# Kernel optimization log

Hardware: AMD Instinct MI355X
Metric: run time of the kernel (lower is better)

The kernel has to match this reference:

```python
import jax, jax.numpy as jnp
import numpy as np

N_FFT = 1024
HOP = 256
WIN = N_FFT  # win_length = n_fft in VocosISTFTHead
PAD = (WIN - HOP) // 2  # 384, 'same' padding trim
CLAMP_MAX = 100.0


def _hann_periodic(n):
    # matches torch.hann_window(n, periodic=True)
    return 0.5 * (1.0 - jnp.cos(2.0 * jnp.pi * jnp.arange(n, dtype=jnp.float32) / n))


def setup_inputs() -> dict:
    key = jax.random.key(0)
    k1, k2, k3 = jax.random.split(key, 3)
    B, T, H = 16, 2048, 512
    hidden_states = jax.random.normal(k1, (B, T, H), dtype=jnp.float32)
    # out_proj: Linear(hidden_dim, n_fft+2); scaled so exp(magnitude) stays sane
    W = jax.random.normal(k2, (N_FFT + 2, H), dtype=jnp.float32) * 0.02
    b = jax.random.normal(k3, (N_FFT + 2,), dtype=jnp.float32) * 0.02
    window = _hann_periodic(WIN)
    return {"hidden_states": hidden_states, "W": W, "b": b, "window": window}


def reference(hidden_states, W, b, window):
    B, T, _ = hidden_states.shape
    # linear projection -> [B, T, n_fft+2] -> transpose -> [B, n_fft+2, T]
    spec = (hidden_states @ W.T + b).transpose(0, 2, 1)
    half = (N_FFT + 2) // 2  # n_fft//2 + 1 = 513 freq bins
    magnitude = jnp.minimum(jnp.exp(spec[:, :half]), CLAMP_MAX)
    phase = spec[:, half:]
    coeffs = magnitude * (jnp.cos(phase) + 1j * jnp.sin(phase))  # [B, F, T] complex
    # inverse rfft along freq axis, norm='backward' (default) -> [B, n_fft, T]
    frames = jnp.fft.irfft(coeffs, n=N_FFT, axis=1)
    frames = frames * window[None, :, None]
    L = (T - 1) * HOP + WIN
    idx = (jnp.arange(T)[:, None] * HOP + jnp.arange(WIN)[None, :]).reshape(-1)
    frames_flat = frames.transpose(0, 2, 1).reshape(B, -1)
    audio = jnp.zeros((B, L), frames.dtype).at[:, idx].add(frames_flat)
    # NOLA normalization: overlap-added squared window
    wsq = jnp.broadcast_to(window ** 2, (T, WIN)).reshape(-1)
    norm = jnp.zeros((L,), window.dtype).at[idx].add(wsq)
    return audio[:, PAD:-PAD] / norm[PAD:-PAD]
```

## Files before the change

### kernel.cpp

```cpp
#include <hip/hip_runtime.h>
#include <hip/hip_fp16.h>
#include <math.h>
#include <stdint.h>


#define FRAMES  32768
#define TWO_PI  6.283185307179586f
#define SPR 4
#define RND 11
#define JB  47

typedef unsigned short ushort_t;
typedef __attribute__((ext_vector_type(8))) _Float16 f16x8;
typedef __attribute__((ext_vector_type(4))) float f32x4;

#define GLDS(gp, lp) __builtin_amdgcn_global_load_lds( \
    (const __attribute__((address_space(1))) void*)(gp), \
    (__attribute__((address_space(3))) void*)(lp), 16, 0, 0)

__device__ __forceinline__ float2 f2(float x, float y){ return make_float2(x,y); }
__device__ __forceinline__ float2 cadd(float2 a, float2 b){ return f2(a.x+b.x, a.y+b.y); }
__device__ __forceinline__ float2 csub(float2 a, float2 b){ return f2(a.x-b.x, a.y-b.y); }
__device__ __forceinline__ float2 cmul(float2 a, float2 b){ return f2(a.x*b.x - a.y*b.y, a.x*b.y + a.y*b.x); }

__device__ __forceinline__ uint32_t pack2h(float a, float b) {
  const ushort_t ha = __half_as_ushort(__float2half_rn(a));
  const ushort_t hb = __half_as_ushort(__float2half_rn(b));
  return (uint32_t)ha | ((uint32_t)hb << 16);
}

__global__ __launch_bounds__(256) void convert_AB(
    const float* __restrict__ hs, const float* __restrict__ Wm,
    const float* __restrict__ bias, ushort_t* __restrict__ Af,
    ushort_t* __restrict__ Whi, __half* __restrict__ coeffs)
{
  const int bid = blockIdx.x;
  const int t = threadIdx.x;
  if (bid < 2048) {
    const int r = t >> 4, c = t & 15;
    const int m = bid * 16 + r;
    const float* src = hs + (size_t)m * 512 + c * 32;
    const float* wm  = Wm + (size_t)512  * 512 + c * 32;
    const float* wp  = Wm + (size_t)1025 * 512 + c * 32;

    float v[32];
    #pragma unroll
    for (int i = 0; i < 8; ++i) *(float4*)&v[i*4] = *(const float4*)(src + i*4);

    float dm = 0.f, dp = 0.f;
    #pragma unroll
    for (int i = 0; i < 8; ++i) {
      const float4 a  = *(const float4*)&v[i*4];
      const float4 m4 = *(const float4*)(wm + i*4);
      const float4 p4 = *(const float4*)(wp + i*4);
      dm = fmaf(a.x,m4.x, fmaf(a.y,m4.y, fmaf(a.z,m4.z, fmaf(a.w,m4.w, dm))));
      dp = fmaf(a.x,p4.x, fmaf(a.y,p4.y, fmaf(a.z,p4.z, fmaf(a.w,p4.w, dp))));
    }

    uint32_t hu[16];
    #pragma unroll
    for (int i = 0; i < 16; ++i) hu[i] = pack2h(v[2*i], v[2*i+1]);
    ushort_t* dh = Af + (size_t)m * 512 + c * 32;
    #pragma unroll
    for (int q = 0; q < 4; ++q)
      *(uint4*)(dh + q*8) = make_uint4(hu[4*q], hu[4*q+1], hu[4*q+2], hu[4*q+3]);

    #pragma unroll
    for (int off = 8; off; off >>= 1) {
      dm += __shfl_xor(dm, off, 16);
      dp += __shfl_xor(dp, off, 16);
    }
    if (c == 0) {
      const float sm = dm + bias[512], sp = dp + bias[1025];
      const float mag = fminf(__expf(sm), 100.0f);
      coeffs[(size_t)m * 1024 + 1] = __float2half_rn(mag * __cosf(sp));
    }
  } else {
    const int gid = (bid - 2048) * 256 + t;
    const int sd = gid & 3;
    const int r  = (gid >> 2) & 255;
    const int kt = (gid >> 10) & 15;
    const int yb = gid >> 14;
    const int srow = (r < 128) ? (yb*128 + r) : (513 + yb*128 + (r - 128));
    const float* src = Wm + (size_t)srow * 512 + kt*32 + sd*8;
    const float4 a = *(const float4*)src;
    const float4 b = *(const float4*)(src + 4);
    const uint4 o = make_uint4(pack2h(a.x,a.y), pack2h(a.z,a.w),
                               pack2h(b.x,b.y), pack2h(b.z,b.w));
    *(uint4*)(Whi + (size_t)gid * 8) = o;
  }
}

__global__ __launch_bounds__(512, 2) void gemm_mfma(
    const ushort_t* __restrict__ Af, const ushort_t* __restrict__ Whi,
    const float* __restrict__ bias, __half* __restrict__ coeffs)
{
  __shared__ ushort_t Ab[24576];

  const int tid = threadIdx.x;
  const int w = tid >> 6, l = tid & 63;
  const int wr = w >> 2, wc = w & 3;
  const int lc = l & 15, kg = l >> 4;

  const int bid = blockIdx.x;
  const int swz = (bid & 7) * 64 + (bid >> 3);
  const int mb = swz >> 2, yb = swz & 3;

  uint32_t pa_off[2], lofs[2];
  #pragma unroll
  for (int ch = 0; ch < 2; ++ch) {
    const int g = ch*512 + tid;
    const int r = g >> 2, sd = g & 3;
    lofs[ch] = r*32 + sd*8;
    const int sl = sd ^ ((r >> 1) & 3);
    pa_off[ch] = (uint32_t)(mb*256 + r)*512 + sl*8;
  }
  uint32_t pb_off[4];
  #pragma unroll
  for (int cf = 0; cf < 4; ++cf) {
    const int rB = ((cf < 2) ? 0 : 128) + wc*32 + (cf & 1)*16 + lc;
    pb_off[cf] = (uint32_t)yb*131072u + rB*32 + kg*8;
  }

  f32x4 acc[8][4];
  #pragma unroll
  for (int rf = 0; rf < 8; ++rf)
    #pragma unroll
    for (int cf = 0; cf < 4; ++cf)
      #pragma unroll
      for (int q = 0; q < 4; ++q) acc[rf][cf][q] = 0.f;

  const int asl = (kg ^ ((lc >> 1) & 3)) * 8;

  f16x8 p[4], q[4];

#define WAITV2 asm volatile("s_waitcnt vmcnt(2) lgkmcnt(0)" ::: "memory")
#define WAITV0 asm volatile("s_waitcnt vmcnt(0) lgkmcnt(0)" ::: "memory")
#define SB     __builtin_amdgcn_s_barrier()
#define SCH0   __builtin_amdgcn_sched_barrier(0)

#define DSREAD(DST, BASE, RF0) do {                                      \
    _Pragma("unroll")                                                    \
    for (int r4 = 0; r4 < 4; ++r4) {                                     \
      const int rr = wr*128 + ((RF0) + r4)*16 + lc;                      \
      DST[r4] = *(const f16x8*)(&Ab[(BASE) + rr*32 + asl]);              \
    }                                                                    \
  } while (0)

#define MFMA16(FA, RF0, RB) do {                                         \
    __builtin_amdgcn_s_setprio(1);                                       \
    _Pragma("unroll")                                                    \
    for (int r4 = 0; r4 < 4; ++r4)                                       \
      _Pragma("unroll")                                                  \
      for (int cf = 0; cf < 4; ++cf)                                     \
        acc[(RF0)+r4][cf] = __builtin_amdgcn_mfma_f32_16x16x32_f16(      \
            FA[r4], RB[cf], acc[(RF0)+r4][cf], 0, 0, 0);                 \
    __builtin_amdgcn_s_setprio(0);                                       \
  } while (0)

#define ITER(KT, RBC, RBN, LAST) do {                                    \
    if (LAST) { WAITV0; } else { WAITV2; }                               \
    SB;                                                                  \
    DSREAD(q, aR, 4);                                                    \
    if ((KT) < 14) GLDS(Af + pa_off[0] + ((KT)+2)*32, &Ab[aW + lofs[0]]);\
    if ((KT) < 15) {                                                     \
      RBN[0] = *(const f16x8*)(Whi + pb_off[0] + ((KT)+1)*8192);         \
      RBN[1] = *(const f16x8*)(Whi + pb_off[1] + ((KT)+1)*8192);         \
    }                                                                    \
    SCH0;                                                                \
    MFMA16(p, 0, RBC);                                                   \
    if ((KT) < 15) DSREAD(p, aN, 0);                                     \
    if ((KT) < 14) GLDS(Af + pa_off[1] + ((KT)+2)*32, &Ab[aW + lofs[1]]);\
    if ((KT) < 15) {                                                     \
      RBN[2] = *(const f16x8*)(Whi + pb_off[2] + ((KT)+1)*8192);         \
      RBN[3] = *(const f16x8*)(Whi + pb_off[3] + ((KT)+1)*8192);         \
    }                                                                    \
    SCH0;                                                                \
    MFMA16(q, 4, RBC);                                                   \
    { const unsigned t_ = aR; aR = aN; aN = aW; aW = t_; }               \
  } while (0)

  f16x8 rb0[4], rb1[4];
  GLDS(Af + pa_off[0], &Ab[lofs[0]]);
  GLDS(Af + pa_off[1], &Ab[lofs[1]]);
  GLDS(Af + pa_off[0] + 32, &Ab[8192 + lofs[0]]);
  GLDS(Af + pa_off[1] + 32, &Ab[8192 + lofs[1]]);
  SCH0;
  #pragma unroll
  for (int j = 0; j < 4; ++j) rb0[j] = *(const f16x8*)(Whi + pb_off[j]);
  SCH0;
  asm volatile("s_waitcnt vmcnt(6)" ::: "memory");
  SB;
  unsigned aR = 0, aN = 8192, aW = 16384;
  DSREAD(p, aR, 0);

  for (int k2 = 0; k2 < 8; ++k2) {
    ITER(2*k2,     rb0, rb1, false);
    ITER(2*k2 + 1, rb1, rb0, k2 == 7);
  }
#undef ITER
#undef DSREAD
#undef MFMA16

  const int pc0 = yb*128 + wc*32 + lc;
  const int pc1 = pc0 + 16;
  const float bm0 = bias[pc0], bp0 = bias[513 + pc0];
  const float bm1 = bias[pc1], bp1 = bias[513 + pc1];
  #pragma unroll
  for (int rf = 0; rf < 8; ++rf) {
    const int rbase = mb*256 + wr*128 + rf*16 + kg*4;
    #pragma unroll
    for (int qi = 0; qi < 4; ++qi) {
      __half* row = coeffs + (size_t)(rbase + qi) * 1024;
      {
        const float sm = acc[rf][0][qi] + bm0;
        const float sp = acc[rf][2][qi] + bp0;
        const float mag = fminf(__expf(sm), 100.0f);
        const float aa = mag * __cosf(sp);
        const float bb = mag * __sinf(sp);
        if (pc0 == 0) row[0] = __float2half_rn(aa);
        else *(__half2*)(row + 2*pc0) = __float22half2_rn(make_float2(aa, bb));
      }
      {
        const float sm = acc[rf][1][qi] + bm1;
        const float sp = acc[rf][3][qi] + bp1;
        const float mag = fminf(__expf(sm), 100.0f);
        const float aa = mag * __cosf(sp);
        const float bb = mag * __sinf(sp);
        *(__half2*)(row + 2*pc1) = __float22half2_rn(make_float2(aa, bb));
      }
    }
  }
}

#define PIDX(s) ((s) + ((s) >> 3))
#define WFENCE  __builtin_amdgcn_wave_barrier()

template<int NS>
__device__ __forceinline__ void stage_fft(const float2* in, float2* out, int l)
{
  float2 v[8];
  #pragma unroll
  for (int r = 0; r < 8; ++r) v[r] = in[PIDX(l + 64*r)];
  if (NS > 1) {
    const float ang = TWO_PI * (float)(l & (NS-1)) / (float)(NS * 8);
    float sn, cs; __sincosf(ang, &sn, &cs);
    const float2 wb = f2(cs, sn);
    float2 cur = wb;
    #pragma unroll
    for (int r = 1; r < 8; ++r) { v[r] = cmul(v[r], cur); cur = cmul(cur, wb); }
  }
  const float2 e0=v[0], e1=v[2], e2=v[4], e3=v[6];
  const float2 o0=v[1], o1=v[3], o2=v[5], o3=v[7];
  float2 a = cadd(e0,e2), b = csub(e0,e2), c = cadd(e1,e3), d = csub(e1,e3);
  const float2 E0 = cadd(a,c), E2 = csub(a,c);
  const float2 E1 = f2(b.x - d.y, b.y + d.x), E3 = f2(b.x + d.y, b.y - d.x);
  a = cadd(o0,o2); b = csub(o0,o2); c = cadd(o1,o3); d = csub(o1,o3);
  const float2 O0 = cadd(a,c), O2 = csub(a,c);
  const float2 O1 = f2(b.x - d.y, b.y + d.x), O3 = f2(b.x + d.y, b.y - d.x);
  const float r2 = 0.70710678118654752f;
  const float2 t0 = O0;
  const float2 t1 = f2(r2*(O1.x - O1.y),  r2*(O1.x + O1.y));
  const float2 t2 = f2(-O2.y, O2.x);
  const float2 t3 = f2(-r2*(O3.x + O3.y), r2*(O3.x - O3.y));
  float2 X[8];
  X[0]=cadd(E0,t0); X[4]=csub(E0,t0);
  X[1]=cadd(E1,t1); X[5]=csub(E1,t1);
  X[2]=cadd(E2,t2); X[6]=csub(E2,t2);
  X[3]=cadd(E3,t3); X[7]=csub(E3,t3);
  const int idxD = (l / NS) * (NS * 8) + (l & (NS-1));
  #pragma unroll
  for (int q = 0; q < 8; ++q) out[PIDX(idxD + q*NS)] = X[q];
}

__device__ __forceinline__ void stage_last(const float2* in, __half* frout,
                                           const float* __restrict__ window, int l)
{
  float2 v[8];
  #pragma unroll
  for (int r = 0; r < 8; ++r) v[r] = in[PIDX(l + 64*r)];
  {
    const float ang = TWO_PI * (float)l / 512.0f;
    float sn, cs; __sincosf(ang, &sn, &cs);
    const float2 wb = f2(cs, sn);
    float2 cur = wb;
    #pragma unroll
    for (int r = 1; r < 8; ++r) { v[r] = cmul(v[r], cur); cur = cmul(cur, wb); }
  }
  const float2 e0=v[0], e1=v[2], e2=v[4], e3=v[6];
  const float2 o0=v[1], o1=v[3], o2=v[5], o3=v[7];
  float2 a = cadd(e0,e2), b = csub(e0,e2), c = cadd(e1,e3), d = csub(e1,e3);
  const float2 E0 = cadd(a,c), E2 = csub(a,c);
  const float2 E1 = f2(b.x - d.y, b.y + d.x), E3 = f2(b.x + d.y, b.y - d.x);
  a = cadd(o0,o2); b = csub(o0,o2); c = cadd(o1,o3); d = csub(o1,o3);
  const float2 O0 = cadd(a,c), O2 = csub(a,c);
  const float2 O1 = f2(b.x - d.y, b.y + d.x), O3 = f2(b.x + d.y, b.y - d.x);
  const float r2 = 0.70710678118654752f;
  const float2 t0 = O0;
  const float2 t1 = f2(r2*(O1.x - O1.y),  r2*(O1.x + O1.y));
  const float2 t2 = f2(-O2.y, O2.x);
  const float2 t3 = f2(-r2*(O3.x + O3.y), r2*(O3.x - O3.y));
  float2 X[8];
  X[0]=cadd(E0,t0); X[4]=csub(E0,t0);
  X[1]=cadd(E1,t1); X[5]=csub(E1,t1);
  X[2]=cadd(E2,t2); X[6]=csub(E2,t2);
  X[3]=cadd(E3,t3); X[7]=csub(E3,t3);
  #pragma unroll
  for (int q = 0; q < 8; ++q) {
    const int m = l + 64*q;
    const float2 wv = *(const float2*)(window + 2*m);
    *(__half2*)&frout[2*m] =
        __float22half2_rn(make_float2(X[q].x * wv.x, X[q].y * wv.y));
  }
}

__device__ __forceinline__ void fft_frame(const __half* __restrict__ cb, int F,
                                          float2* bAw, float2* bBw,
                                          __half (*fr)[1024],
                                          const float* __restrict__ window, int l)
{
  if (F < 0 || F > 2047) return;
  const __half2* crow = (const __half2*)(cb + (size_t)F * 1024);
  const float sc = 1.0f / 1024.0f;
  #pragma unroll
  for (int jj = 0; jj < 4; ++jj) {
    const int k = 1 + l + 64*jj;
    const float2 Ck = __half22float2(crow[k]);
    const float2 Cq = __half22float2(crow[512-k]);
    float sn, cs; __sincosf(TWO_PI * (1.0f/1024.0f) * (float)k, &sn, &cs);
    const float Ex = sc*(Ck.x + Cq.x), Ey = sc*(Ck.y - Cq.y);
    const float Dx = Ck.x - Cq.x,      Dy = Ck.y + Cq.y;
    const float Ox = sc*(cs*Dx - sn*Dy), Oy = sc*(cs*Dy + sn*Dx);
    bAw[PIDX(k)]     = f2(Ex - Oy, Ey + Ox);
    bAw[PIDX(512-k)] = f2(Ex + Oy, Ox - Ey);
  }
  if (l == 0) {
    const float2 dn = __half22float2(crow[0]);
    bAw[PIDX(0)] = f2(sc*(dn.x + dn.y), sc*(dn.x - dn.y));
  }
  WFENCE;
  stage_fft<1>(bAw, bBw, l);
  WFENCE;
  stage_fft<8>(bBw, bAw, l);
  WFENCE;
  stage_last(bAw, fr[F & 7], window, l);
  WFENCE;
}

__global__ __launch_bounds__(256) void fft_oa(
    const __half* __restrict__ coeffs, const float* __restrict__ window,
    float* __restrict__ out)
{
  __shared__ float2 bA[4][576];
  __shared__ float2 bB[4][576];
  __shared__ __half fr[8][1024];

  const int tid = threadIdx.x;
  const int w = tid >> 6, l = tid & 63;
  const int bid = blockIdx.x;
  const int b = bid / JB, j = bid - b * JB;
  const int T0 = SPR * RND * j;

  const __half* cb = coeffs + (size_t)b * 2048 * 1024;
  float* outb = out + (size_t)b * 524288;

  float wsq[4];
  #pragma unroll
  for (int i = 0; i < 4; ++i) {
    const float wv = window[tid + 256*i];
    wsq[i] = wv * wv;
  }

  if (w < 3) fft_frame(cb, T0 - 3 + w, bA[w], bB[w], fr, window, l);

  for (int r = 0; r < RND; ++r) {
    fft_frame(cb, T0 + SPR*r + w, bA[w], bB[w], fr, window, l);
    __syncthreads();
    #pragma unroll
    for (int k = 0; k < SPR; ++k) {
      const int s = T0 + SPR*r + k;
      const int o = 256*s + tid - 384;
      float acc = 0.f, nrm = 0.f;
      #pragma unroll
      for (int i = 0; i < 4; ++i) {
        const int f = s - i;
        if (f >= 0 && f <= 2047) {
          acc += __half2float(fr[f & 7][tid + 256*i]);
          nrm += wsq[i];
        }
      }
      if (o >= 0 && o < 524288) outb[o] = acc / nrm;
    }
    __syncthreads();
  }
}

extern "C" void kernel_launch(void* const* d_in, const int* in_sizes, int n_in,
                              void* d_out, int out_size, void* d_ws, size_t ws_size,
                              hipStream_t stream)
{
  const float* hs     = (const float*)d_in[0];
  const float* Wm     = (const float*)d_in[1];
  const float* bias   = (const float*)d_in[2];
  const float* window = (const float*)d_in[3];

  char* base = (char*)d_ws;
  ushort_t* Af     = (ushort_t*)base;
  ushort_t* Whi    = (ushort_t*)(base + 33554432);
  __half*   coeffs = (__half*)(base + 67108864);

  convert_AB<<<2304, 256, 0, stream>>>(hs, Wm, bias, Af, Whi, coeffs);
  gemm_mfma<<<512,  512, 0, stream>>>(Af, Whi, bias, coeffs);
  fft_oa<<<16 * JB, 256, 0, stream>>>(coeffs, window, (float*)d_out);
}
```

Baseline: 133.2 us.

## Prefetch next frame coefficients into registers and precompute FFT twiddles

Splits the per-frame FFT into a coefficient load and a processing step, so each wave issues the global loads for its next frame before running the current frame's FFT stages, giving register double-buffering. Twiddle factors for the pre-twist and the radix-8 stages are computed once per thread at kernel start rather than with sincos inside every frame. The block decomposition also changes from 11 to 8 rounds, with more blocks per batch. This raises register pressure from the twiddle and prefetch arrays, and shorter blocks recompute proportionally more halo frames.

```diff
diff --git a/kernel.cpp b/kernel.cpp
--- a/kernel.cpp
+++ b/kernel.cpp
@@ -7,8 +7,8 @@
 #define FRAMES  32768
 #define TWO_PI  6.283185307179586f
 #define SPR 4
-#define RND 11
-#define JB  47
+#define RND 8
+#define JB  65
 
 typedef unsigned short ushort_t;
 typedef __attribute__((ext_vector_type(8))) _Float16 f16x8;
@@ -237,18 +237,15 @@
 #define WFENCE  __builtin_amdgcn_wave_barrier()
 
 template<int NS>
-__device__ __forceinline__ void stage_fft(const float2* in, float2* out, int l)
+__device__ __forceinline__ void stage_fft(const float2* in, float2* out, int l,
+                                          const float2* pw)
 {
   float2 v[8];
   #pragma unroll
   for (int r = 0; r < 8; ++r) v[r] = in[PIDX(l + 64*r)];
   if (NS > 1) {
-    const float ang = TWO_PI * (float)(l & (NS-1)) / (float)(NS * 8);
-    float sn, cs; __sincosf(ang, &sn, &cs);
-    const float2 wb = f2(cs, sn);
-    float2 cur = wb;
-    #pragma unroll
-    for (int r = 1; r < 8; ++r) { v[r] = cmul(v[r], cur); cur = cmul(cur, wb); }
+    #pragma unroll
+    for (int r = 1; r < 8; ++r) v[r] = cmul(v[r], pw[r-1]);
   }
   const float2 e0=v[0], e1=v[2], e2=v[4], e3=v[6];
   const float2 o0=v[1], o1=v[3], o2=v[5], o3=v[7];
@@ -274,19 +271,14 @@
 }
 
 __device__ __forceinline__ void stage_last(const float2* in, __half* frout,
-                                           const float* __restrict__ window, int l)
+                                           const float* __restrict__ window, int l,
+                                           const float2* pw)
 {
   float2 v[8];
   #pragma unroll
   for (int r = 0; r < 8; ++r) v[r] = in[PIDX(l + 64*r)];
-  {
-    const float ang = TWO_PI * (float)l / 512.0f;
-    float sn, cs; __sincosf(ang, &sn, &cs);
-    const float2 wb = f2(cs, sn);
-    float2 cur = wb;
-    #pragma unroll
-    for (int r = 1; r < 8; ++r) { v[r] = cmul(v[r], cur); cur = cmul(cur, wb); }
-  }
+  #pragma unroll
+  for (int r = 1; r < 8; ++r) v[r] = cmul(v[r], pw[r-1]);
   const float2 e0=v[0], e1=v[2], e2=v[4], e3=v[6];
   const float2 o0=v[1], o1=v[3], o2=v[5], o3=v[7];
   float2 a = cadd(e0,e2), b = csub(e0,e2), c = cadd(e1,e3), d = csub(e1,e3);
@@ -314,36 +306,54 @@
   }
 }
 
-__device__ __forceinline__ void fft_frame(const __half* __restrict__ cb, int F,
-                                          float2* bAw, float2* bBw,
-                                          __half (*fr)[1024],
-                                          const float* __restrict__ window, int l)
+__device__ __forceinline__ void load_coef(const __half* __restrict__ cb, int F,
+                                          int l, uint32_t* ld)
 {
   if (F < 0 || F > 2047) return;
-  const __half2* crow = (const __half2*)(cb + (size_t)F * 1024);
-  const float sc = 1.0f / 1024.0f;
+  const uint32_t* crow = (const uint32_t*)(cb + (size_t)F * 1024);
   #pragma unroll
   for (int jj = 0; jj < 4; ++jj) {
     const int k = 1 + l + 64*jj;
-    const float2 Ck = __half22float2(crow[k]);
-    const float2 Cq = __half22float2(crow[512-k]);
-    float sn, cs; __sincosf(TWO_PI * (1.0f/1024.0f) * (float)k, &sn, &cs);
-    const float Ex = sc*(Ck.x + Cq.x), Ey = sc*(Ck.y - Cq.y);
-    const float Dx = Ck.x - Cq.x,      Dy = Ck.y + Cq.y;
-    const float Ox = sc*(cs*Dx - sn*Dy), Oy = sc*(cs*Dy + sn*Dx);
-    bAw[PIDX(k)]     = f2(Ex - Oy, Ey + Ox);
-    bAw[PIDX(512-k)] = f2(Ex + Oy, Ox - Ey);
-  }
-  if (l == 0) {
-    const float2 dn = __half22float2(crow[0]);
-    bAw[PIDX(0)] = f2(sc*(dn.x + dn.y), sc*(dn.x - dn.y));
-  }
+    ld[2*jj]   = crow[k];
+    ld[2*jj+1] = crow[512-k];
+  }
+  ld[8] = crow[0];
+}
+
+__device__ __forceinline__ void proc_frame(
+    const uint32_t* ld, int F, const __half* __restrict__ cb, int Fn,
+    uint32_t* ldn, float2* bAw, float2* bBw, __half (*fr)[1024],
+    const float2* twp, const float2* pw8, const float2* pwL,
+    const float* __restrict__ window, int l)
+{
+  const float sc = 1.0f / 1024.0f;
+  const bool valid = (F >= 0 && F <= 2047);
+  if (valid) {
+    #pragma unroll
+    for (int jj = 0; jj < 4; ++jj) {
+      const int k = 1 + l + 64*jj;
+      const float2 Ck = __half22float2(*(const __half2*)&ld[2*jj]);
+      const float2 Cq = __half22float2(*(const __half2*)&ld[2*jj+1]);
+      const float cs = twp[jj].x, sn = twp[jj].y;
+      const float Ex = sc*(Ck.x + Cq.x), Ey = sc*(Ck.y - Cq.y);
+      const float Dx = Ck.x - Cq.x,      Dy = Ck.y + Cq.y;
+      const float Ox = sc*(cs*Dx - sn*Dy), Oy = sc*(cs*Dy + sn*Dx);
+      bAw[PIDX(k)]     = f2(Ex - Oy, Ey + Ox);
+      bAw[PIDX(512-k)] = f2(Ex + Oy, Ox - Ey);
+    }
+    if (l == 0) {
+      const float2 dn = __half22float2(*(const __half2*)&ld[8]);
+      bAw[PIDX(0)] = f2(sc*(dn.x + dn.y), sc*(dn.x - dn.y));
+    }
+  }
+  load_coef(cb, Fn, l, ldn);
+  if (!valid) return;
   WFENCE;
-  stage_fft<1>(bAw, bBw, l);
+  stage_fft<1>(bAw, bBw, l, pw8);
   WFENCE;
-  stage_fft<8>(bBw, bAw, l);
+  stage_fft<8>(bBw, bAw, l, pw8);
   WFENCE;
-  stage_last(bAw, fr[F & 7], window, l);
+  stage_last(bAw, fr[F & 7], window, l, pwL);
   WFENCE;
 }
 
@@ -364,6 +374,27 @@
   const __half* cb = coeffs + (size_t)b * 2048 * 1024;
   float* outb = out + (size_t)b * 524288;
 
+  float2 twp[4], pw8[7], pwL[7];
+  #pragma unroll
+  for (int jj = 0; jj < 4; ++jj) {
+    float sn, cs;
+    __sincosf(TWO_PI * (1.0f/1024.0f) * (float)(1 + l + 64*jj), &sn, &cs);
+    twp[jj] = f2(cs, sn);
+  }
+  {
+    const float a8 = TWO_PI * (float)(l & 7) / 64.0f;
+    const float aL = TWO_PI * (float)l / 512.0f;
+    #pragma unroll
+    for (int r = 1; r < 8; ++r) {
+      float sn, cs;
+      __sincosf(a8 * (float)r, &sn, &cs); pw8[r-1] = f2(cs, sn);
+    }
+    #pragma unroll
+    for (int r = 1; r < 8; ++r) {
+      float sn, cs;
+      __sincosf(aL * (float)r, &sn, &cs); pwL[r-1] = f2(cs, sn);
+    }
+  }
   float wsq[4];
   #pragma unroll
   for (int i = 0; i < 4; ++i) {
@@ -371,10 +402,19 @@
     wsq[i] = wv * wv;
   }
 
-  if (w < 3) fft_frame(cb, T0 - 3 + w, bA[w], bB[w], fr, window, l);
-
+  uint32_t lda[9], ldb[9];
+  const int Fp = (w < 3) ? (T0 - 3 + w) : -1;
+  load_coef(cb, Fp, l, lda);
+  proc_frame(lda, Fp, cb, T0 + w, ldb, bA[w], bB[w], fr, twp, pw8, pwL, window, l);
+
+  #pragma unroll
   for (int r = 0; r < RND; ++r) {
-    fft_frame(cb, T0 + SPR*r + w, bA[w], bB[w], fr, window, l);
+    const int F  = T0 + SPR*r + w;
+    const int Fn = (r + 1 < RND) ? (F + SPR) : -1;
+    if ((r & 1) == 0)
+      proc_frame(ldb, F, cb, Fn, lda, bA[w], bB[w], fr, twp, pw8, pwL, window, l);
+    else
+      proc_frame(lda, F, cb, Fn, ldb, bA[w], bB[w], fr, twp, pw8, pwL, window, l);
     __syncthreads();
     #pragma unroll
     for (int k = 0; k < SPR; ++k) {
```

Measured after the change: 139.6 us. 4.8% more time.
